# Kernel tuning notes

Hardware: AMD Instinct MI355X
Metric: run time of the kernel (lower is better)

## Reference

```python
import jax, jax.numpy as jnp
import numpy as np

N = 2048          # num nodes
C = 256           # dense_dim per input
EMB = 3 * C       # 768
H = 8             # num_heads
D = EMB // H      # 96 head_dim
ALPHA = 0.2       # leaky relu slope
SCALE = D ** -0.5


def setup_inputs() -> dict:
    key = jax.random.key(0)
    ks = jax.random.split(key, 9)
    sd = EMB ** -0.5
    return {
        "eh": jax.random.normal(ks[0], (N, C), jnp.float32),
        "er": jax.random.normal(ks[1], (N, C), jnp.float32),
        "et": jax.random.normal(ks[2], (N, C), jnp.float32),
        "h_id": jax.random.randint(ks[3], (N,), 0, 32),
        "W_w": jax.random.normal(ks[4], (EMB, EMB), jnp.float32) * sd,
        "a": jax.random.normal(ks[5], (2 * D, 1), jnp.float32) * (2 * D) ** -0.5,
        "proj_w": jax.random.normal(ks[6], (EMB, EMB), jnp.float32) * sd,
        "proj_b": jnp.zeros((EMB,), jnp.float32),
        "skip_w": jax.random.normal(ks[7], (EMB, EMB), jnp.float32) * sd,
        "skip_b": jnp.zeros((EMB,), jnp.float32),
    }


def reference(eh, er, et, h_id, W_w, a, proj_w, proj_b, skip_w, skip_b):
    n = eh.shape[0]
    e = jnp.concatenate([eh, er, et], axis=-1)            # [N, EMB]
    Wh = (e @ W_w.T).reshape(n, H, D)                     # [N, H, D]

    # score = leakyrelu(a1 . Wh_scrambled[i] + a2 . Wh[j]) * scale
    a1, a2 = a[:D, 0], a[D:, 0]
    s1 = Wh @ a1                                          # [N, H]
    s2 = Wh @ a2                                          # [N, H]
    # torch's Wh.repeat(1,1,N).view(N*N,H,D) reads head (j*H + h)//N for pair (i,j,h)
    qidx = (jnp.arange(n)[:, None] * H + jnp.arange(H)[None, :]) // n  # [N, H]
    x = s1[:, qidx] + s2[None, :, :]                      # [N, N, H]
    e_ij = jnp.where(x >= 0, x, ALPHA * x) * SCALE

    mask = h_id[:, None] != h_id[None, :]                 # [N, N]
    e_ij = jnp.where(mask[:, :, None], -jnp.inf, e_ij)
    attn = jax.nn.softmax(e_ij, axis=1)                   # softmax over neighbors j

    out = jnp.einsum('ijh,jhd->ihd', attn, Wh).reshape(n, H * D)
    out = out @ proj_w.T + proj_b                         # [N, EMB]
    skip = e @ skip_w.T + skip_b                          # [N, EMB]
    return skip + out
```

## Files before the change

kernel.cpp:

```cpp
#include <hip/hip_runtime.h>
#include <hip/hip_bf16.h>

#define N_NODES 2048
#define EMB 768
#define NH 8
#define DH 96
#define ALPHA 0.2f
#define SCALE 0.10206207261596575f
#define NGMAX 192
#define WSZ (EMB * EMB)

typedef __bf16 bf16x8 __attribute__((ext_vector_type(8)));
typedef float f32x4 __attribute__((ext_vector_type(4)));
typedef __attribute__((address_space(3))) unsigned int lds_u32;
typedef __attribute__((address_space(1))) const unsigned int glb_u32;

union pack4 { ushort4 u; __hip_bfloat16 h[4]; };

__global__ __launch_bounds__(256) void prep_kernel(
    const float* __restrict__ eh, const float* __restrict__ er, const float* __restrict__ et,
    const float* __restrict__ W0, const float* __restrict__ W1, const float* __restrict__ W2,
    __hip_bfloat16* __restrict__ e, __hip_bfloat16* __restrict__ o0,
    __hip_bfloat16* __restrict__ o1, __hip_bfloat16* __restrict__ o2, int* __restrict__ cnt)
{
    const int b = blockIdx.x;
    const int gtid = b * 256 + threadIdx.x;
    if (gtid < 32) cnt[gtid] = 0;
    const float* src;
    __hip_bfloat16* dst;
    if (b < 1536) {
        int idx = gtid * 4;
        int i = idx / EMB, c = idx % EMB;
        if (c < 256)      src = eh + i * 256 + c;
        else if (c < 512) src = er + i * 256 + (c - 256);
        else              src = et + i * 256 + (c - 512);
        dst = e + (size_t)i * EMB + c;
    } else {
        int idx = (gtid - 1536 * 256) * 4;
        if (idx < WSZ)          { src = W0 + idx;           dst = o0 + idx; }
        else if (idx < 2 * WSZ) { src = W1 + idx - WSZ;     dst = o1 + idx - WSZ; }
        else                    { src = W2 + idx - 2 * WSZ; dst = o2 + idx - 2 * WSZ; }
    }
    float4 v = *reinterpret_cast<const float4*>(src);
    pack4 p;
    p.h[0] = __float2bfloat16(v.x);
    p.h[1] = __float2bfloat16(v.y);
    p.h[2] = __float2bfloat16(v.z);
    p.h[3] = __float2bfloat16(v.w);
    *reinterpret_cast<ushort4*>(dst) = p.u;
}

__device__ __forceinline__ void stage128(
    const __hip_bfloat16* __restrict__ src, int row0, int k0,
    __hip_bfloat16* lds, int wave, int lane)
{
#pragma unroll
    for (int i = 0; i < 4; i++) {
        const int c0 = wave * 256 + i * 64;
        const int c = c0 + lane;
        const int row = c >> 4;
        const int cb = (c & 15) ^ (row & 15);
        const __hip_bfloat16* g = src + (size_t)(row0 + row) * EMB + k0 + cb * 8;
        __builtin_amdgcn_global_load_lds((glb_u32*)g, (lds_u32*)(lds + c0 * 8), 16, 0, 0);
    }
}

__global__ __launch_bounds__(256) void gemm_nt_kernel(
    const __hip_bfloat16* __restrict__ A1, const __hip_bfloat16* __restrict__ B1, int ns1,
    const __hip_bfloat16* __restrict__ A2, const __hip_bfloat16* __restrict__ B2, int ns2,
    const float* __restrict__ bias1, const float* __restrict__ bias2,
    float* __restrict__ Cf)
{
    __shared__ __attribute__((aligned(16))) __hip_bfloat16 sm[2][2][8192];

    const int t = threadIdx.x;
    const int lane = t & 63, wave = t >> 6;
    const int wm = wave >> 1, wn = wave & 1;
    const int bm = blockIdx.y * 64, bn = blockIdx.x * 64;
    const int l15 = lane & 15, quad = lane >> 4;
    const int NS = ns1 + ns2;
    const int rA = wm * 32 + l15, rB = wn * 32 + l15;

    f32x4 acc00 = {0.f,0.f,0.f,0.f}, acc01 = {0.f,0.f,0.f,0.f};
    f32x4 acc10 = {0.f,0.f,0.f,0.f}, acc11 = {0.f,0.f,0.f,0.f};

    stage128(A1, bm, 0, &sm[0][0][0], wave, lane);
    stage128(B1, bn, 0, &sm[0][1][0], wave, lane);

    for (int s = 0; s < NS; s++) {
        __syncthreads();
        if (s + 1 < NS) {
            const int sn = s + 1;
            const __hip_bfloat16* As = (sn < ns1) ? A1 : A2;
            const __hip_bfloat16* Bs = (sn < ns1) ? B1 : B2;
            const int k0 = ((sn < ns1) ? sn : sn - ns1) * 128;
            stage128(As, bm, k0, &sm[sn & 1][0][0], wave, lane);
            stage128(Bs, bn, k0, &sm[sn & 1][1][0], wave, lane);
        }
        const __hip_bfloat16* At = &sm[s & 1][0][0];
        const __hip_bfloat16* Bt = &sm[s & 1][1][0];
#pragma unroll
        for (int ks = 0; ks < 4; ks++) {
            const int cq = ks * 4 + quad;
            bf16x8 a0 = *(const bf16x8*)(At + (size_t)(rA * 16        + (cq ^ l15)) * 8);
            bf16x8 a1 = *(const bf16x8*)(At + (size_t)((rA + 16) * 16 + (cq ^ l15)) * 8);
            bf16x8 b0 = *(const bf16x8*)(Bt + (size_t)(rB * 16        + (cq ^ l15)) * 8);
            bf16x8 b1 = *(const bf16x8*)(Bt + (size_t)((rB + 16) * 16 + (cq ^ l15)) * 8);
            acc00 = __builtin_amdgcn_mfma_f32_16x16x32_bf16(a0, b0, acc00, 0, 0, 0);
            acc01 = __builtin_amdgcn_mfma_f32_16x16x32_bf16(a0, b1, acc01, 0, 0, 0);
            acc10 = __builtin_amdgcn_mfma_f32_16x16x32_bf16(a1, b0, acc10, 0, 0, 0);
            acc11 = __builtin_amdgcn_mfma_f32_16x16x32_bf16(a1, b1, acc11, 0, 0, 0);
        }
    }

    const int col0 = bn + wn * 32 + l15;
    const int col1 = col0 + 16;
    float bv0 = 0.f, bv1 = 0.f;
    if (bias1 != nullptr) {
        bv0 = bias1[col0] + bias2[col0];
        bv1 = bias1[col1] + bias2[col1];
    }
    const int r0 = bm + wm * 32 + quad * 4;
#pragma unroll
    for (int r = 0; r < 4; r++) {
        const int row0 = r0 + r, row1 = r0 + 16 + r;
        Cf[(size_t)row0 * EMB + col0] = acc00[r] + bv0;
        Cf[(size_t)row0 * EMB + col1] = acc01[r] + bv1;
        Cf[(size_t)row1 * EMB + col0] = acc10[r] + bv0;
        Cf[(size_t)row1 * EMB + col1] = acc11[r] + bv1;
    }
}

__global__ __launch_bounds__(256) void s12g_kernel(
    const float* __restrict__ Wh, const float* __restrict__ a,
    float* __restrict__ s1, float* __restrict__ s2,
    const int* __restrict__ h_id, int* __restrict__ cnt, int* __restrict__ lists)
{
    int gid = blockIdx.x * 256 + threadIdx.x;
    if (gid < N_NODES) {
        int g = h_id[gid];
        int p = atomicAdd(&cnt[g], 1);
        lists[g * N_NODES + p] = gid;
    }
    int i = gid >> 3, h = gid & 7;
    const float* wr = Wh + (size_t)i * EMB + h * DH;
    float acc1 = 0.f, acc2 = 0.f;
    for (int d = 0; d < DH; d++) {
        float w = wr[d];
        acc1 += w * a[d];
        acc2 += w * a[DH + d];
    }
    s1[gid] = acc1;
    s2[gid] = acc2;
}

__global__ __launch_bounds__(256) void attn_kernel(
    const float* __restrict__ Wh, const float* __restrict__ s1, const float* __restrict__ s2,
    const int* __restrict__ cnt, const int* __restrict__ lists,
    __hip_bfloat16* __restrict__ out)
{
    const int g  = blockIdx.x & 31;
    const int h  = (blockIdx.x >> 5) & 7;
    const int dh = blockIdx.x >> 8;
    const int t  = threadIdx.x;

    __shared__ int   jb[NGMAX];
    __shared__ int   qg[NGMAX];
    __shared__ float s2g[NGMAX];
    __shared__ float s1g[NGMAX][9];
    __shared__ float Whg[NGMAX][48];

    const int ng = min(cnt[g], NGMAX);
    const int* gl = lists + g * N_NODES;

    for (int j = t; j < ng; j += 256) {
        int node = gl[j];
        jb[j]  = node;
        qg[j]  = node >> 8;
        s2g[j] = s2[node * 8 + h];
        float4 v0 = *reinterpret_cast<const float4*>(s1 + node * 8);
        float4 v1 = *reinterpret_cast<const float4*>(s1 + node * 8 + 4);
        s1g[j][0] = v0.x; s1g[j][1] = v0.y; s1g[j][2] = v0.z; s1g[j][3] = v0.w;
        s1g[j][4] = v1.x; s1g[j][5] = v1.y; s1g[j][6] = v1.z; s1g[j][7] = v1.w;
    }
    __syncthreads();
    for (int idx = t; idx < ng * 12; idx += 256) {
        int jc = idx / 12, dq = idx % 12;
        float4 v = *reinterpret_cast<const float4*>(
            Wh + (size_t)jb[jc] * EMB + h * DH + dh * 48 + dq * 4);
        *reinterpret_cast<float4*>(&Whg[jc][dq * 4]) = v;
    }
    __syncthreads();

    if (t < ng) {
        float m = -1e30f;
        for (int j = 0; j < ng; j++) {
            float x = s1g[t][qg[j]] + s2g[j];
            float ev = (x >= 0.f ? x : ALPHA * x) * SCALE;
            m = fmaxf(m, ev);
        }
        float S = 0.f;
        for (int j = 0; j < ng; j++) {
            float x = s1g[t][qg[j]] + s2g[j];
            float ev = (x >= 0.f ? x : ALPHA * x) * SCALE;
            S += __expf(ev - m);
        }
        const float ri = 1.f / S;

        float acc[48];
#pragma unroll
        for (int d = 0; d < 48; d++) acc[d] = 0.f;
        for (int j = 0; j < ng; j++) {
            float x = s1g[t][qg[j]] + s2g[j];
            float ev = (x >= 0.f ? x : ALPHA * x) * SCALE;
            float p = __expf(ev - m) * ri;
#pragma unroll
            for (int d = 0; d < 48; d++) acc[d] += p * Whg[j][d];
        }
        __hip_bfloat16* po = out + (size_t)jb[t] * EMB + h * DH + dh * 48;
#pragma unroll
        for (int d = 0; d < 48; d += 4) {
            pack4 pk;
            pk.h[0] = __float2bfloat16(acc[d]);
            pk.h[1] = __float2bfloat16(acc[d + 1]);
            pk.h[2] = __float2bfloat16(acc[d + 2]);
            pk.h[3] = __float2bfloat16(acc[d + 3]);
            *reinterpret_cast<ushort4*>(po + d) = pk.u;
        }
    }
}

extern "C" void kernel_launch(void* const* d_in, const int* in_sizes, int n_in,
                              void* d_out, int out_size, void* d_ws, size_t ws_size,
                              hipStream_t stream)
{
    const float* eh     = (const float*)d_in[0];
    const float* er     = (const float*)d_in[1];
    const float* et     = (const float*)d_in[2];
    const int*   h_id   = (const int*)d_in[3];
    const float* W_w    = (const float*)d_in[4];
    const float* a      = (const float*)d_in[5];
    const float* proj_w = (const float*)d_in[6];
    const float* proj_b = (const float*)d_in[7];
    const float* skip_w = (const float*)d_in[8];
    const float* skip_b = (const float*)d_in[9];
    float* out = (float*)d_out;

    char* ws = (char*)d_ws;
    __hip_bfloat16* e_ws   = (__hip_bfloat16*)(ws);
    float*          Wh_ws  = (float*)(ws + 3145728);
    __hip_bfloat16* at_ws  = (__hip_bfloat16*)(ws + 9437184);
    __hip_bfloat16* Wb_ws  = (__hip_bfloat16*)(ws + 12582912);
    __hip_bfloat16* Pb_ws  = (__hip_bfloat16*)(ws + 13762560);
    __hip_bfloat16* Sb_ws  = (__hip_bfloat16*)(ws + 14942208);
    float*          s1_ws  = (float*)(ws + 16121856);
    float*          s2_ws  = (float*)(ws + 16187392);
    int*            cnt_ws = (int*)(ws + 16252928);
    int*            lst_ws = (int*)(ws + 16253056);

    prep_kernel<<<3264, 256, 0, stream>>>(eh, er, et, W_w, proj_w, skip_w,
                                          e_ws, Wb_ws, Pb_ws, Sb_ws, cnt_ws);

    gemm_nt_kernel<<<dim3(12, 32), 256, 0, stream>>>(
        e_ws, Wb_ws, 6, nullptr, nullptr, 0, nullptr, nullptr, Wh_ws);

    s12g_kernel<<<64, 256, 0, stream>>>(Wh_ws, a, s1_ws, s2_ws, h_id, cnt_ws, lst_ws);

    attn_kernel<<<512, 256, 0, stream>>>(Wh_ws, s1_ws, s2_ws, cnt_ws, lst_ws, at_ws);

    gemm_nt_kernel<<<dim3(12, 32), 256, 0, stream>>>(
        at_ws, Pb_ws, 6, e_ws, Sb_ws, 6, proj_b, skip_b, out);
}
```

Before: 136.7 us.

## Fuse skip GEMM into first GEMM sharing A tile, retile to 64x48

The skip projection (e @ skip_w^T + biases) moves into the first GEMM, which now computes Wh and skip together from one shared staged A tile. The output GEMM then only does attn @ proj_w^T and accumulates into the output with a read-modify-write. Tiles change from 64x64 to 64x48 with one 16-row strip per wave, raising the grid to 16x32 blocks. This cuts redundant loads of e and gives more blocks, at the cost of an extra read of out and lower MFMA reuse per A fragment in the second GEMM.

```diff
diff --git a/kernel.cpp b/kernel.cpp
--- a/kernel.cpp
+++ b/kernel.cpp
@@ -50,84 +50,148 @@
     *reinterpret_cast<ushort4*>(dst) = p.u;
 }
 
-__device__ __forceinline__ void stage128(
-    const __hip_bfloat16* __restrict__ src, int row0, int k0,
-    __hip_bfloat16* lds, int wave, int lane)
-{
-#pragma unroll
-    for (int i = 0; i < 4; i++) {
-        const int c0 = wave * 256 + i * 64;
-        const int c = c0 + lane;
-        const int row = c >> 4;
-        const int cb = (c & 15) ^ (row & 15);
-        const __hip_bfloat16* g = src + (size_t)(row0 + row) * EMB + k0 + cb * 8;
-        __builtin_amdgcn_global_load_lds((glb_u32*)g, (lds_u32*)(lds + c0 * 8), 16, 0, 0);
-    }
-}
-
-__global__ __launch_bounds__(256) void gemm_nt_kernel(
-    const __hip_bfloat16* __restrict__ A1, const __hip_bfloat16* __restrict__ B1, int ns1,
-    const __hip_bfloat16* __restrict__ A2, const __hip_bfloat16* __restrict__ B2, int ns2,
-    const float* __restrict__ bias1, const float* __restrict__ bias2,
-    float* __restrict__ Cf)
-{
-    __shared__ __attribute__((aligned(16))) __hip_bfloat16 sm[2][2][8192];
+
+__global__ __launch_bounds__(256) void gemm1_kernel(
+    const __hip_bfloat16* __restrict__ A, const __hip_bfloat16* __restrict__ BW,
+    const __hip_bfloat16* __restrict__ BS,
+    const float* __restrict__ pb, const float* __restrict__ sb,
+    float* __restrict__ Wh, float* __restrict__ out)
+{
+    __shared__ __attribute__((aligned(16))) __hip_bfloat16 smA[2][8192];
+    __shared__ __attribute__((aligned(16))) __hip_bfloat16 smW[2][6144];
+    __shared__ __attribute__((aligned(16))) __hip_bfloat16 smS[2][6144];
 
     const int t = threadIdx.x;
     const int lane = t & 63, wave = t >> 6;
-    const int wm = wave >> 1, wn = wave & 1;
-    const int bm = blockIdx.y * 64, bn = blockIdx.x * 64;
     const int l15 = lane & 15, quad = lane >> 4;
-    const int NS = ns1 + ns2;
-    const int rA = wm * 32 + l15, rB = wn * 32 + l15;
-
-    f32x4 acc00 = {0.f,0.f,0.f,0.f}, acc01 = {0.f,0.f,0.f,0.f};
-    f32x4 acc10 = {0.f,0.f,0.f,0.f}, acc11 = {0.f,0.f,0.f,0.f};
-
-    stage128(A1, bm, 0, &sm[0][0][0], wave, lane);
-    stage128(B1, bn, 0, &sm[0][1][0], wave, lane);
-
-    for (int s = 0; s < NS; s++) {
+    const int bm = blockIdx.y * 64, bn = blockIdx.x * 48;
+
+    f32x4 aW[3], aS[3];
+#pragma unroll
+    for (int fc = 0; fc < 3; fc++) { aW[fc] = (f32x4){0,0,0,0}; aS[fc] = (f32x4){0,0,0,0}; }
+
+    auto stage = [&](int k0, int bi) {
+#pragma unroll
+        for (int i = 0; i < 4; i++) {
+            int L = t + i * 256, row = L >> 4, cb = (L & 15) ^ (row & 15);
+            __builtin_amdgcn_global_load_lds(
+                (glb_u32*)(A + (size_t)(bm + row) * EMB + k0 + cb * 8),
+                (lds_u32*)(&smA[bi][0] + L * 8), 16, 0, 0);
+        }
+#pragma unroll
+        for (int i = 0; i < 3; i++) {
+            int L = t + i * 256, row = L >> 4, cb = (L & 15) ^ (row & 15);
+            __builtin_amdgcn_global_load_lds(
+                (glb_u32*)(BW + (size_t)(bn + row) * EMB + k0 + cb * 8),
+                (lds_u32*)(&smW[bi][0] + L * 8), 16, 0, 0);
+        }
+#pragma unroll
+        for (int i = 0; i < 3; i++) {
+            int L = t + i * 256, row = L >> 4, cb = (L & 15) ^ (row & 15);
+            __builtin_amdgcn_global_load_lds(
+                (glb_u32*)(BS + (size_t)(bn + row) * EMB + k0 + cb * 8),
+                (lds_u32*)(&smS[bi][0] + L * 8), 16, 0, 0);
+        }
+    };
+
+    stage(0, 0);
+    const int rA = wave * 16 + l15;
+    for (int s = 0; s < 6; s++) {
         __syncthreads();
-        if (s + 1 < NS) {
-            const int sn = s + 1;
-            const __hip_bfloat16* As = (sn < ns1) ? A1 : A2;
-            const __hip_bfloat16* Bs = (sn < ns1) ? B1 : B2;
-            const int k0 = ((sn < ns1) ? sn : sn - ns1) * 128;
-            stage128(As, bm, k0, &sm[sn & 1][0][0], wave, lane);
-            stage128(Bs, bn, k0, &sm[sn & 1][1][0], wave, lane);
-        }
-        const __hip_bfloat16* At = &sm[s & 1][0][0];
-        const __hip_bfloat16* Bt = &sm[s & 1][1][0];
+        if (s < 5) stage((s + 1) * 128, (s + 1) & 1);
+        const __hip_bfloat16* At = smA[s & 1];
+        const __hip_bfloat16* Wt = smW[s & 1];
+        const __hip_bfloat16* St = smS[s & 1];
 #pragma unroll
         for (int ks = 0; ks < 4; ks++) {
             const int cq = ks * 4 + quad;
-            bf16x8 a0 = *(const bf16x8*)(At + (size_t)(rA * 16        + (cq ^ l15)) * 8);
-            bf16x8 a1 = *(const bf16x8*)(At + (size_t)((rA + 16) * 16 + (cq ^ l15)) * 8);
-            bf16x8 b0 = *(const bf16x8*)(Bt + (size_t)(rB * 16        + (cq ^ l15)) * 8);
-            bf16x8 b1 = *(const bf16x8*)(Bt + (size_t)((rB + 16) * 16 + (cq ^ l15)) * 8);
-            acc00 = __builtin_amdgcn_mfma_f32_16x16x32_bf16(a0, b0, acc00, 0, 0, 0);
-            acc01 = __builtin_amdgcn_mfma_f32_16x16x32_bf16(a0, b1, acc01, 0, 0, 0);
-            acc10 = __builtin_amdgcn_mfma_f32_16x16x32_bf16(a1, b0, acc10, 0, 0, 0);
-            acc11 = __builtin_amdgcn_mfma_f32_16x16x32_bf16(a1, b1, acc11, 0, 0, 0);
-        }
-    }
-
-    const int col0 = bn + wn * 32 + l15;
-    const int col1 = col0 + 16;
-    float bv0 = 0.f, bv1 = 0.f;
-    if (bias1 != nullptr) {
-        bv0 = bias1[col0] + bias2[col0];
-        bv1 = bias1[col1] + bias2[col1];
-    }
-    const int r0 = bm + wm * 32 + quad * 4;
-#pragma unroll
-    for (int r = 0; r < 4; r++) {
-        const int row0 = r0 + r, row1 = r0 + 16 + r;
-        Cf[(size_t)row0 * EMB + col0] = acc00[r] + bv0;
-        Cf[(size_t)row0 * EMB + col1] = acc01[r] + bv1;
-        Cf[(size_t)row1 * EMB + col0] = acc10[r] + bv0;
-        Cf[(size_t)row1 * EMB + col1] = acc11[r] + bv1;
+            bf16x8 a = *(const bf16x8*)(At + (size_t)((rA << 4) + (cq ^ (rA & 15))) * 8);
+#pragma unroll
+            for (int fc = 0; fc < 3; fc++) {
+                const int rB = fc * 16 + l15;
+                bf16x8 bw = *(const bf16x8*)(Wt + (size_t)((rB << 4) + (cq ^ (rB & 15))) * 8);
+                bf16x8 bs = *(const bf16x8*)(St + (size_t)((rB << 4) + (cq ^ (rB & 15))) * 8);
+                aW[fc] = __builtin_amdgcn_mfma_f32_16x16x32_bf16(a, bw, aW[fc], 0, 0, 0);
+                aS[fc] = __builtin_amdgcn_mfma_f32_16x16x32_bf16(a, bs, aS[fc], 0, 0, 0);
+            }
+        }
+    }
+
+    const int r0 = bm + wave * 16 + quad * 4;
+#pragma unroll
+    for (int fc = 0; fc < 3; fc++) {
+        const int col = bn + fc * 16 + l15;
+        const float bv = pb[col] + sb[col];
+#pragma unroll
+        for (int r = 0; r < 4; r++) {
+            Wh[(size_t)(r0 + r) * EMB + col]  = aW[fc][r];
+            out[(size_t)(r0 + r) * EMB + col] = aS[fc][r] + bv;
+        }
+    }
+}
+
+__global__ __launch_bounds__(256) void gemm2_kernel(
+    const __hip_bfloat16* __restrict__ A, const __hip_bfloat16* __restrict__ B,
+    float* __restrict__ out)
+{
+    __shared__ __attribute__((aligned(16))) __hip_bfloat16 smA[2][8192];
+    __shared__ __attribute__((aligned(16))) __hip_bfloat16 smB[2][6144];
+
+    const int t = threadIdx.x;
+    const int lane = t & 63, wave = t >> 6;
+    const int l15 = lane & 15, quad = lane >> 4;
+    const int bm = blockIdx.y * 64, bn = blockIdx.x * 48;
+
+    f32x4 acc[3];
+#pragma unroll
+    for (int fc = 0; fc < 3; fc++) acc[fc] = (f32x4){0, 0, 0, 0};
+
+    auto stage = [&](int k0, int bi) {
+#pragma unroll
+        for (int i = 0; i < 4; i++) {
+            int L = t + i * 256, row = L >> 4, cb = (L & 15) ^ (row & 15);
+            __builtin_amdgcn_global_load_lds(
+                (glb_u32*)(A + (size_t)(bm + row) * EMB + k0 + cb * 8),
+                (lds_u32*)(&smA[bi][0] + L * 8), 16, 0, 0);
+        }
+#pragma unroll
+        for (int i = 0; i < 3; i++) {
+            int L = t + i * 256, row = L >> 4, cb = (L & 15) ^ (row & 15);
+            __builtin_amdgcn_global_load_lds(
+                (glb_u32*)(B + (size_t)(bn + row) * EMB + k0 + cb * 8),
+                (lds_u32*)(&smB[bi][0] + L * 8), 16, 0, 0);
+        }
+    };
+
+    stage(0, 0);
+    const int rA = wave * 16 + l15;
+    for (int s = 0; s < 6; s++) {
+        __syncthreads();
+        if (s < 5) stage((s + 1) * 128, (s + 1) & 1);
+        const __hip_bfloat16* At = smA[s & 1];
+        const __hip_bfloat16* Bt = smB[s & 1];
+#pragma unroll
+        for (int ks = 0; ks < 4; ks++) {
+            const int cq = ks * 4 + quad;
+            bf16x8 a = *(const bf16x8*)(At + (size_t)((rA << 4) + (cq ^ (rA & 15))) * 8);
+#pragma unroll
+            for (int fc = 0; fc < 3; fc++) {
+                const int rB = fc * 16 + l15;
+                bf16x8 b = *(const bf16x8*)(Bt + (size_t)((rB << 4) + (cq ^ (rB & 15))) * 8);
+                acc[fc] = __builtin_amdgcn_mfma_f32_16x16x32_bf16(a, b, acc[fc], 0, 0, 0);
+            }
+        }
+    }
+
+    const int r0 = bm + wave * 16 + quad * 4;
+#pragma unroll
+    for (int fc = 0; fc < 3; fc++) {
+        const int col = bn + fc * 16 + l15;
+#pragma unroll
+        for (int r = 0; r < 4; r++) {
+            float* p = &out[(size_t)(r0 + r) * EMB + col];
+            *p = *p + acc[fc][r];
+        }
     }
 }
 
@@ -261,13 +325,12 @@
     prep_kernel<<<3264, 256, 0, stream>>>(eh, er, et, W_w, proj_w, skip_w,
                                           e_ws, Wb_ws, Pb_ws, Sb_ws, cnt_ws);
 
-    gemm_nt_kernel<<<dim3(12, 32), 256, 0, stream>>>(
-        e_ws, Wb_ws, 6, nullptr, nullptr, 0, nullptr, nullptr, Wh_ws);
+    gemm1_kernel<<<dim3(16, 32), 256, 0, stream>>>(
+        e_ws, Wb_ws, Sb_ws, proj_b, skip_b, Wh_ws, out);
 
     s12g_kernel<<<64, 256, 0, stream>>>(Wh_ws, a, s1_ws, s2_ws, h_id, cnt_ws, lst_ws);
 
     attn_kernel<<<512, 256, 0, stream>>>(Wh_ws, s1_ws, s2_ws, cnt_ws, lst_ws, at_ws);
 
-    gemm_nt_kernel<<<dim3(12, 32), 256, 0, stream>>>(
-        at_ws, Pb_ws, 6, e_ws, Sb_ws, 6, proj_b, skip_b, out);
-}
+    gemm2_kernel<<<dim3(16, 32), 256, 0, stream>>>(at_ws, Pb_ws, out);
+}
```

After: 141.6 us. +3.6%, slower.

## Fold score dot-products into attention kernel and group build into GEMM

Applied to the files above, without the earlier changes.

Removes the separate s1/s2 scoring kernel. The h_id group-list construction moves into the first GEMM's prologue, and each attention block now computes the s1 and s2 head scores for its group members directly from Wh. This saves one launch and a dependent small-kernel stage. In exchange, each of the 512 attention blocks redundantly recomputes the dot products for all 8 heads of every group member, which adds global reads and ALU work per block.

```diff
diff --git a/kernel.cpp b/kernel.cpp
--- a/kernel.cpp
+++ b/kernel.cpp
@@ -69,7 +69,8 @@
     const __hip_bfloat16* __restrict__ A1, const __hip_bfloat16* __restrict__ B1, int ns1,
     const __hip_bfloat16* __restrict__ A2, const __hip_bfloat16* __restrict__ B2, int ns2,
     const float* __restrict__ bias1, const float* __restrict__ bias2,
-    float* __restrict__ Cf)
+    float* __restrict__ Cf,
+    const int* __restrict__ h_id, int* __restrict__ cnt, int* __restrict__ lists)
 {
     __shared__ __attribute__((aligned(16))) __hip_bfloat16 sm[2][2][8192];
 
@@ -80,6 +81,15 @@
     const int l15 = lane & 15, quad = lane >> 4;
     const int NS = ns1 + ns2;
     const int rA = wm * 32 + l15, rB = wn * 32 + l15;
+
+    if (h_id != nullptr) {
+        int fid = (blockIdx.y * 12 + blockIdx.x) * 256 + t;
+        if (fid < N_NODES) {
+            int g = h_id[fid];
+            int p = atomicAdd(&cnt[g], 1);
+            lists[g * N_NODES + p] = fid;
+        }
+    }
 
     f32x4 acc00 = {0.f,0.f,0.f,0.f}, acc01 = {0.f,0.f,0.f,0.f};
     f32x4 acc10 = {0.f,0.f,0.f,0.f}, acc11 = {0.f,0.f,0.f,0.f};
@@ -131,31 +141,8 @@
     }
 }
 
-__global__ __launch_bounds__(256) void s12g_kernel(
-    const float* __restrict__ Wh, const float* __restrict__ a,
-    float* __restrict__ s1, float* __restrict__ s2,
-    const int* __restrict__ h_id, int* __restrict__ cnt, int* __restrict__ lists)
-{
-    int gid = blockIdx.x * 256 + threadIdx.x;
-    if (gid < N_NODES) {
-        int g = h_id[gid];
-        int p = atomicAdd(&cnt[g], 1);
-        lists[g * N_NODES + p] = gid;
-    }
-    int i = gid >> 3, h = gid & 7;
-    const float* wr = Wh + (size_t)i * EMB + h * DH;
-    float acc1 = 0.f, acc2 = 0.f;
-    for (int d = 0; d < DH; d++) {
-        float w = wr[d];
-        acc1 += w * a[d];
-        acc2 += w * a[DH + d];
-    }
-    s1[gid] = acc1;
-    s2[gid] = acc2;
-}
-
 __global__ __launch_bounds__(256) void attn_kernel(
-    const float* __restrict__ Wh, const float* __restrict__ s1, const float* __restrict__ s2,
+    const float* __restrict__ Wh, const float* __restrict__ av,
     const int* __restrict__ cnt, const int* __restrict__ lists,
     __hip_bfloat16* __restrict__ out)
 {
@@ -165,25 +152,54 @@
     const int t  = threadIdx.x;
 
     __shared__ int   jb[NGMAX];
-    __shared__ int   qg[NGMAX];
     __shared__ float s2g[NGMAX];
     __shared__ float s1g[NGMAX][9];
     __shared__ float Whg[NGMAX][48];
+    __shared__ float a1s[96], a2s[96];
+    __shared__ int   qg[NGMAX];
 
     const int ng = min(cnt[g], NGMAX);
     const int* gl = lists + g * N_NODES;
 
+    if (t < 96)                a1s[t]      = av[t];
+    else if (t < 192)          a2s[t - 96] = av[t];
     for (int j = t; j < ng; j += 256) {
         int node = gl[j];
-        jb[j]  = node;
-        qg[j]  = node >> 8;
-        s2g[j] = s2[node * 8 + h];
-        float4 v0 = *reinterpret_cast<const float4*>(s1 + node * 8);
-        float4 v1 = *reinterpret_cast<const float4*>(s1 + node * 8 + 4);
-        s1g[j][0] = v0.x; s1g[j][1] = v0.y; s1g[j][2] = v0.z; s1g[j][3] = v0.w;
-        s1g[j][4] = v1.x; s1g[j][5] = v1.y; s1g[j][6] = v1.z; s1g[j][7] = v1.w;
+        jb[j] = node;
+        qg[j] = node >> 8;
     }
     __syncthreads();
+
+    {
+        const int q = t & 3;
+        const float* a1q = a1s;
+        for (int j0 = 0; j0 < ng; j0 += 64) {
+            const int j = j0 + (t >> 2);
+            if (j < ng) {
+                const float* w = Wh + (size_t)jb[j] * EMB + q * 192;
+                float d0 = 0.f, d1 = 0.f;
+#pragma unroll
+                for (int d = 0; d < 96; d += 4) {
+                    float4 u = *reinterpret_cast<const float4*>(w + d);
+                    float4 v = *reinterpret_cast<const float4*>(w + 96 + d);
+                    d0 += u.x * a1q[d] + u.y * a1q[d + 1] + u.z * a1q[d + 2] + u.w * a1q[d + 3];
+                    d1 += v.x * a1q[d] + v.y * a1q[d + 1] + v.z * a1q[d + 2] + v.w * a1q[d + 3];
+                }
+                s1g[j][2 * q]     = d0;
+                s1g[j][2 * q + 1] = d1;
+                if ((h >> 1) == q) {
+                    const float* ws = w + (h & 1) * 96;
+                    float d2 = 0.f;
+#pragma unroll
+                    for (int d = 0; d < 96; d += 4) {
+                        float4 u = *reinterpret_cast<const float4*>(ws + d);
+                        d2 += u.x * a2s[d] + u.y * a2s[d + 1] + u.z * a2s[d + 2] + u.w * a2s[d + 3];
+                    }
+                    s2g[j] = d2;
+                }
+            }
+        }
+    }
     for (int idx = t; idx < ng * 12; idx += 256) {
         int jc = idx / 12, dq = idx % 12;
         float4 v = *reinterpret_cast<const float4*>(
@@ -253,8 +269,6 @@
     __hip_bfloat16* Wb_ws  = (__hip_bfloat16*)(ws + 12582912);
     __hip_bfloat16* Pb_ws  = (__hip_bfloat16*)(ws + 13762560);
     __hip_bfloat16* Sb_ws  = (__hip_bfloat16*)(ws + 14942208);
-    float*          s1_ws  = (float*)(ws + 16121856);
-    float*          s2_ws  = (float*)(ws + 16187392);
     int*            cnt_ws = (int*)(ws + 16252928);
     int*            lst_ws = (int*)(ws + 16253056);
 
@@ -262,12 +276,12 @@
                                           e_ws, Wb_ws, Pb_ws, Sb_ws, cnt_ws);
 
     gemm_nt_kernel<<<dim3(12, 32), 256, 0, stream>>>(
-        e_ws, Wb_ws, 6, nullptr, nullptr, 0, nullptr, nullptr, Wh_ws);
-
-    s12g_kernel<<<64, 256, 0, stream>>>(Wh_ws, a, s1_ws, s2_ws, h_id, cnt_ws, lst_ws);
-
-    attn_kernel<<<512, 256, 0, stream>>>(Wh_ws, s1_ws, s2_ws, cnt_ws, lst_ws, at_ws);
+        e_ws, Wb_ws, 6, nullptr, nullptr, 0, nullptr, nullptr, Wh_ws,
+        h_id, cnt_ws, lst_ws);
+
+    attn_kernel<<<512, 256, 0, stream>>>(Wh_ws, a, cnt_ws, lst_ws, at_ws);
 
     gemm_nt_kernel<<<dim3(12, 32), 256, 0, stream>>>(
-        at_ws, Pb_ws, 6, e_ws, Sb_ws, 6, proj_b, skip_b, out);
-}
+        at_ws, Pb_ws, 6, e_ws, Sb_ws, 6, proj_b, skip_b, out,
+        nullptr, nullptr, nullptr);
+}
```

New measurement: 161.5 us. 18.2% more time.

## Split attention head dim across all four waves and move grouping into GEMM

Applied to the files above, without the earlier changes.

Previously only threads with t < ng (at most 192 of 256, about one wave's worth for ~64-node groups) did the attention work, each accumulating 48 outputs. Now each of the four waves takes a 12-column slice of the 48-wide head chunk, and lanes loop over query nodes in steps of 64. This spreads the weighted-sum work across all waves and cuts the accumulator from 48 to 12 registers per thread. The cost is that each wave recomputes the softmax max and sum on its own. The group-list building, which uses atomics on h_id, moves from the s1/s2 kernel into the first GEMM's prologue, so the small s12 kernel no longer does it.

```diff
diff --git a/kernel.cpp b/kernel.cpp
--- a/kernel.cpp
+++ b/kernel.cpp
@@ -69,7 +69,8 @@
     const __hip_bfloat16* __restrict__ A1, const __hip_bfloat16* __restrict__ B1, int ns1,
     const __hip_bfloat16* __restrict__ A2, const __hip_bfloat16* __restrict__ B2, int ns2,
     const float* __restrict__ bias1, const float* __restrict__ bias2,
-    float* __restrict__ Cf)
+    float* __restrict__ Cf,
+    const int* __restrict__ h_id, int* __restrict__ cnt, int* __restrict__ lists)
 {
     __shared__ __attribute__((aligned(16))) __hip_bfloat16 sm[2][2][8192];
 
@@ -80,6 +81,15 @@
     const int l15 = lane & 15, quad = lane >> 4;
     const int NS = ns1 + ns2;
     const int rA = wm * 32 + l15, rB = wn * 32 + l15;
+
+    if (h_id != nullptr) {
+        int fid = (blockIdx.y * 12 + blockIdx.x) * 256 + t;
+        if (fid < N_NODES) {
+            int g = h_id[fid];
+            int p = atomicAdd(&cnt[g], 1);
+            lists[g * N_NODES + p] = fid;
+        }
+    }
 
     f32x4 acc00 = {0.f,0.f,0.f,0.f}, acc01 = {0.f,0.f,0.f,0.f};
     f32x4 acc10 = {0.f,0.f,0.f,0.f}, acc11 = {0.f,0.f,0.f,0.f};
@@ -131,17 +141,11 @@
     }
 }
 
-__global__ __launch_bounds__(256) void s12g_kernel(
+__global__ __launch_bounds__(256) void s12_kernel(
     const float* __restrict__ Wh, const float* __restrict__ a,
-    float* __restrict__ s1, float* __restrict__ s2,
-    const int* __restrict__ h_id, int* __restrict__ cnt, int* __restrict__ lists)
+    float* __restrict__ s1, float* __restrict__ s2)
 {
     int gid = blockIdx.x * 256 + threadIdx.x;
-    if (gid < N_NODES) {
-        int g = h_id[gid];
-        int p = atomicAdd(&cnt[g], 1);
-        lists[g * N_NODES + p] = gid;
-    }
     int i = gid >> 3, h = gid & 7;
     const float* wr = Wh + (size_t)i * EMB + h * DH;
     float acc1 = 0.f, acc2 = 0.f;
@@ -163,6 +167,7 @@
     const int h  = (blockIdx.x >> 5) & 7;
     const int dh = blockIdx.x >> 8;
     const int t  = threadIdx.x;
+    const int lane = t & 63, wv = t >> 6;
 
     __shared__ int   jb[NGMAX];
     __shared__ int   qg[NGMAX];
@@ -192,40 +197,42 @@
     }
     __syncthreads();
 
-    if (t < ng) {
-        float m = -1e30f;
-        for (int j = 0; j < ng; j++) {
-            float x = s1g[t][qg[j]] + s2g[j];
-            float ev = (x >= 0.f ? x : ALPHA * x) * SCALE;
-            m = fmaxf(m, ev);
-        }
-        float S = 0.f;
-        for (int j = 0; j < ng; j++) {
-            float x = s1g[t][qg[j]] + s2g[j];
-            float ev = (x >= 0.f ? x : ALPHA * x) * SCALE;
-            S += __expf(ev - m);
-        }
-        const float ri = 1.f / S;
-
-        float acc[48];
-#pragma unroll
-        for (int d = 0; d < 48; d++) acc[d] = 0.f;
-        for (int j = 0; j < ng; j++) {
-            float x = s1g[t][qg[j]] + s2g[j];
-            float ev = (x >= 0.f ? x : ALPHA * x) * SCALE;
-            float p = __expf(ev - m) * ri;
-#pragma unroll
-            for (int d = 0; d < 48; d++) acc[d] += p * Whg[j][d];
-        }
-        __hip_bfloat16* po = out + (size_t)jb[t] * EMB + h * DH + dh * 48;
-#pragma unroll
-        for (int d = 0; d < 48; d += 4) {
-            pack4 pk;
-            pk.h[0] = __float2bfloat16(acc[d]);
-            pk.h[1] = __float2bfloat16(acc[d + 1]);
-            pk.h[2] = __float2bfloat16(acc[d + 2]);
-            pk.h[3] = __float2bfloat16(acc[d + 3]);
-            *reinterpret_cast<ushort4*>(po + d) = pk.u;
+    for (int n0 = 0; n0 < ng; n0 += 64) {
+        const int tn = n0 + lane;
+        if (tn < ng) {
+            float m = -1e30f;
+            for (int j = 0; j < ng; j++) {
+                float x = s1g[tn][qg[j]] + s2g[j];
+                float ev = (x >= 0.f ? x : ALPHA * x) * SCALE;
+                m = fmaxf(m, ev);
+            }
+            float S = 0.f;
+            for (int j = 0; j < ng; j++) {
+                float x = s1g[tn][qg[j]] + s2g[j];
+                float ev = (x >= 0.f ? x : ALPHA * x) * SCALE;
+                S += __expf(ev - m);
+            }
+            const float ri = 1.f / S;
+            float acc[12];
+#pragma unroll
+            for (int d = 0; d < 12; d++) acc[d] = 0.f;
+            for (int j = 0; j < ng; j++) {
+                float x = s1g[tn][qg[j]] + s2g[j];
+                float ev = (x >= 0.f ? x : ALPHA * x) * SCALE;
+                float p = __expf(ev - m) * ri;
+#pragma unroll
+                for (int d = 0; d < 12; d++) acc[d] += p * Whg[j][wv * 12 + d];
+            }
+            __hip_bfloat16* po = out + (size_t)jb[tn] * EMB + h * DH + dh * 48 + wv * 12;
+#pragma unroll
+            for (int d = 0; d < 12; d += 4) {
+                pack4 pk;
+                pk.h[0] = __float2bfloat16(acc[d]);
+                pk.h[1] = __float2bfloat16(acc[d + 1]);
+                pk.h[2] = __float2bfloat16(acc[d + 2]);
+                pk.h[3] = __float2bfloat16(acc[d + 3]);
+                *reinterpret_cast<ushort4*>(po + d) = pk.u;
+            }
         }
     }
 }
@@ -262,12 +269,14 @@
                                           e_ws, Wb_ws, Pb_ws, Sb_ws, cnt_ws);
 
     gemm_nt_kernel<<<dim3(12, 32), 256, 0, stream>>>(
-        e_ws, Wb_ws, 6, nullptr, nullptr, 0, nullptr, nullptr, Wh_ws);
-
-    s12g_kernel<<<64, 256, 0, stream>>>(Wh_ws, a, s1_ws, s2_ws, h_id, cnt_ws, lst_ws);
+        e_ws, Wb_ws, 6, nullptr, nullptr, 0, nullptr, nullptr, Wh_ws,
+        h_id, cnt_ws, lst_ws);
+
+    s12_kernel<<<64, 256, 0, stream>>>(Wh_ws, a, s1_ws, s2_ws);
 
     attn_kernel<<<512, 256, 0, stream>>>(Wh_ws, s1_ws, s2_ws, cnt_ws, lst_ws, at_ws);
 
     gemm_nt_kernel<<<dim3(12, 32), 256, 0, stream>>>(
-        at_ws, Pb_ws, 6, e_ws, Sb_ws, 6, proj_b, skip_b, out);
-}
+        at_ws, Pb_ws, 6, e_ws, Sb_ws, 6, proj_b, skip_b, out,
+        nullptr, nullptr, nullptr);
+}
```

After: 145.6 us. 6.5% more time.
